# Kernel optimization log

Hardware: AMD Instinct MI355X
Metric: run time of the kernel (lower is better)

Reference implementation:

```python
import jax, jax.numpy as jnp
import numpy as np

N = 100000
E = 1600000
F = 64
THETA = (0.6, -0.4, 0.3, -0.2, 0.1)  # k = 5 polynomial coefficients


def setup_inputs() -> dict:
    key = jax.random.key(0)
    kx, ke = jax.random.split(key)
    x = jax.random.normal(kx, (N, F), dtype=jnp.float32)
    edge_index = jax.random.randint(ke, (2, E), 0, N, dtype=jnp.int64)
    return {"x": x, "edge_index": edge_index}


def _l_sym_mul(feat, src, dst, deg_inv_sqrt, n):
    # L_sym * feat = feat - D^{-1/2} A D^{-1/2} feat
    src_norm = feat[src] * deg_inv_sqrt[src]            # [E, F] gather + scale
    agg = jax.ops.segment_sum(src_norm, dst, num_segments=n)  # scatter-add to dst
    return feat - deg_inv_sqrt * agg


def reference(x, edge_index):
    src, dst = edge_index[0], edge_index[1]
    n = x.shape[0]
    # in-degree from dst, clamp to >= 1, D^{-1/2} as [N, 1]
    deg = jax.ops.segment_sum(jnp.ones((src.shape[0],), dtype=x.dtype), dst,
                              num_segments=n)
    deg = jnp.maximum(deg, 1.0)[:, None]
    deg_inv_sqrt = deg ** -0.5

    h_acc = THETA[0] * x
    feat = x
    for k in range(1, len(THETA)):
        feat = _l_sym_mul(feat, src, dst, deg_inv_sqrt, n)
        h_acc = h_acc + THETA[k] * feat
    return h_acc
```

## Files before the change

### kernel.cpp

```cpp
#include <hip/hip_runtime.h>


constexpr int kF = 64;
constexpr int BSHIFT = 8;
constexpr int NB = 1 << BSHIFT;
constexpr int TILE = 4096;
constexpr int KMAX = 512;

static __device__ __forceinline__ float bfl(unsigned u) {
    return __uint_as_float(u << 16);
}
static __device__ __forceinline__ float bfh(unsigned u) {
    return __uint_as_float(u & 0xffff0000u);
}
static __device__ __forceinline__ unsigned f2bf(float f) {
    unsigned u = __float_as_uint(f);
    return (u + 0x7fffu + ((u >> 16) & 1u)) >> 16;
}
static __device__ __forceinline__ unsigned pack2(float a, float b) {
    return f2bf(a) | (f2bf(b) << 16);
}

__global__ void k_binA(const int* __restrict__ src, const int* __restrict__ dst,
                       unsigned* __restrict__ pairs, int* __restrict__ gcursor,
                       const float4* __restrict__ x4, uint4* __restrict__ xb4,
                       int n8, int E, int K, int cap) {
    __shared__ int hist[KMAX];
    __shared__ int gb[KMAX];
    const int tid = threadIdx.x;
    const long long tb = (long long)blockIdx.x * TILE;
    const int tcount = (int)min((long long)TILE, (long long)E - tb);

    {
        int per = (n8 + gridDim.x - 1) / (int)gridDim.x;
        int b0 = blockIdx.x * per;
        int b1 = min(b0 + per, n8);
        for (int i = b0 + tid; i < b1; i += 512) {
            float4 a = x4[2 * i];
            float4 b = x4[2 * i + 1];
            uint4 o;
            o.x = pack2(a.x, a.y);
            o.y = pack2(a.z, a.w);
            o.z = pack2(b.x, b.y);
            o.w = pack2(b.z, b.w);
            xb4[i] = o;
        }
    }

    hist[tid] = 0;
    __syncthreads();
    for (int i = tid; i < tcount; i += 512)
        atomicAdd(&hist[dst[tb + i] >> BSHIFT], 1);
    __syncthreads();
    int hv = hist[tid];
    gb[tid] = (tid < K && hv > 0) ? atomicAdd(&gcursor[tid], hv) : 0;
    hist[tid] = 0;
    __syncthreads();
    for (int i = tid; i < tcount; i += 512) {
        int d = dst[tb + i];
        int s = src[tb + i];
        int b = d >> BSHIFT;
        int pos = atomicAdd(&hist[b], 1);
        pairs[(size_t)b * cap + gb[b] + pos] =
            ((unsigned)(d & (NB - 1)) << 23) | (unsigned)s;
    }
}

__global__ void k_binB1(const unsigned* __restrict__ pairs, const int* __restrict__ gcursor,
                        int* __restrict__ rp, float* __restrict__ dinv,
                        int N, int E, int K, int cap) {
    __shared__ int gsc[KMAX];
    __shared__ int cnt[NB];
    __shared__ int stmp[NB];
    const int b = blockIdx.x;
    const int tid = threadIdx.x;

    int gv = (tid < K) ? gcursor[tid] : 0;
    gsc[tid] = gv;
    __syncthreads();
    for (int o = 1; o < KMAX; o <<= 1) {
        int t = (tid >= o) ? gsc[tid - o] : 0;
        __syncthreads();
        gsc[tid] += t;
        __syncthreads();
    }
    const int ecnt = gcursor[b];
    const int base = gsc[b] - ecnt;
    const unsigned* bp = pairs + (size_t)b * cap;

    if (tid < NB) cnt[tid] = 0;
    __syncthreads();
    for (int i = tid; i < ecnt; i += 512)
        atomicAdd(&cnt[bp[i] >> 23], 1);
    __syncthreads();
    int v = (tid < NB) ? cnt[tid] : 0;
    if (tid < NB) stmp[tid] = v;
    __syncthreads();
    for (int o = 1; o < NB; o <<= 1) {
        int t = (tid >= o && tid < NB) ? stmp[tid - o] : 0;
        __syncthreads();
        if (tid < NB) stmp[tid] += t;
        __syncthreads();
    }
    int node = (b << BSHIFT) + tid;
    if (tid < NB && node < N) {
        rp[node] = base + stmp[tid] - v;
        dinv[node] = rsqrtf(fmaxf((float)v, 1.0f));
    }
    if (b == K - 1 && tid == 0) rp[N] = E;
}

__global__ void k_binB2(const unsigned* __restrict__ pairs, const int* __restrict__ gcursor,
                        const int* __restrict__ rp, const float* __restrict__ dinv,
                        int2* __restrict__ ecsr, int N, int K, int cap) {
    __shared__ int cur[NB];
    const int b = blockIdx.x;
    const int tid = threadIdx.x;
    const int ecnt = gcursor[b];
    const unsigned* bp = pairs + (size_t)b * cap;

    int node = (b << BSHIFT) + tid;
    if (tid < NB) cur[tid] = (node < N) ? rp[node] : 0;
    __syncthreads();
    for (int i = tid; i < ecnt; i += 512) {
        unsigned p = bp[i];
        int s = (int)(p & 0x7FFFFFu);
        int pos = atomicAdd(&cur[p >> 23], 1);
        ecsr[pos] = make_int2(s, __float_as_int(dinv[s]));
    }
}

__global__ void k_gather(const int* __restrict__ rp, const int2* __restrict__ ecsr,
                         const unsigned short* __restrict__ featin,
                         const float* __restrict__ dinv,
                         unsigned short* __restrict__ featout, int n) {
    int wid = (blockIdx.x * blockDim.x + threadIdx.x) >> 6;
    int lane = threadIdx.x & 63;
    int half = lane >> 5;
    int r = (lane >> 3) & 3;
    int c = lane & 7;
    int node = wid * 2 + half;
    if (wid * 2 >= n) return;
    bool valid = node < n;
    int beg = valid ? rp[node] : 0;
    int end = valid ? rp[node + 1] : 0;
    int len = end - beg;
    int olen = __shfl_xor(len, 32, 64);
    int mlen = (len > olen) ? len : olen;

    float acc[8] = {0.f, 0.f, 0.f, 0.f, 0.f, 0.f, 0.f, 0.f};
    for (int i = 0; i < mlen; i += 8) {
        int j1 = beg + i + r;
        int j2 = j1 + 4;
        bool ok1 = j1 < end;
        bool ok2 = j2 < end;
        int2 e1 = ecsr[ok1 ? j1 : 0];
        int2 e2 = ecsr[ok2 ? j2 : 0];
        int s1 = e1.x;
        int s2 = e2.x;
        float w1 = ok1 ? __int_as_float(e1.y) : 0.0f;
        float w2 = ok2 ? __int_as_float(e2.y) : 0.0f;
        uint4 ra = *(const uint4*)(featin + ((size_t)s1 << 6) + (c << 3));
        uint4 rb = *(const uint4*)(featin + ((size_t)s2 << 6) + (c << 3));
        acc[0] += w1 * bfl(ra.x);
        acc[1] += w1 * bfh(ra.x);
        acc[2] += w1 * bfl(ra.y);
        acc[3] += w1 * bfh(ra.y);
        acc[4] += w1 * bfl(ra.z);
        acc[5] += w1 * bfh(ra.z);
        acc[6] += w1 * bfl(ra.w);
        acc[7] += w1 * bfh(ra.w);
        acc[0] += w2 * bfl(rb.x);
        acc[1] += w2 * bfh(rb.x);
        acc[2] += w2 * bfl(rb.y);
        acc[3] += w2 * bfh(rb.y);
        acc[4] += w2 * bfl(rb.z);
        acc[5] += w2 * bfh(rb.z);
        acc[6] += w2 * bfl(rb.w);
        acc[7] += w2 * bfh(rb.w);
    }
    #pragma unroll
    for (int m = 8; m <= 16; m <<= 1) {
        #pragma unroll
        for (int i = 0; i < 8; ++i)
            acc[i] += __shfl_xor(acc[i], m, 64);
    }

    if (r == 0 && valid) {
        size_t off = ((size_t)node << 6) + (c << 3);
        uint4 rr = *(const uint4*)(featin + off);
        float di = dinv[node];
        uint4 o;
        o.x = pack2(bfl(rr.x) - di * acc[0], bfh(rr.x) - di * acc[1]);
        o.y = pack2(bfl(rr.y) - di * acc[2], bfh(rr.y) - di * acc[3]);
        o.z = pack2(bfl(rr.z) - di * acc[4], bfh(rr.z) - di * acc[5]);
        o.w = pack2(bfl(rr.w) - di * acc[6], bfh(rr.w) - di * acc[7]);
        *(uint4*)(featout + off) = o;
    }
}

__global__ void k_final(const float4* __restrict__ x4,
                        const uint4* __restrict__ f1, const uint4* __restrict__ f2,
                        const uint4* __restrict__ f3, const uint4* __restrict__ f4,
                        float4* __restrict__ h4, int n8,
                        float t0, float t1, float t2, float t3, float t4) {
    int i = blockIdx.x * blockDim.x + threadIdx.x;
    if (i >= n8) return;
    uint4 a = f1[i], b = f2[i], cc = f3[i], d = f4[i];
    float4 xa = x4[2 * i], xb = x4[2 * i + 1];
    float4 h0, h1;
    h0.x = t0 * xa.x + t1 * bfl(a.x) + t2 * bfl(b.x) + t3 * bfl(cc.x) + t4 * bfl(d.x);
    h0.y = t0 * xa.y + t1 * bfh(a.x) + t2 * bfh(b.x) + t3 * bfh(cc.x) + t4 * bfh(d.x);
    h0.z = t0 * xa.z + t1 * bfl(a.y) + t2 * bfl(b.y) + t3 * bfl(cc.y) + t4 * bfl(d.y);
    h0.w = t0 * xa.w + t1 * bfh(a.y) + t2 * bfh(b.y) + t3 * bfh(cc.y) + t4 * bfh(d.y);
    h1.x = t0 * xb.x + t1 * bfl(a.z) + t2 * bfl(b.z) + t3 * bfl(cc.z) + t4 * bfl(d.z);
    h1.y = t0 * xb.y + t1 * bfh(a.z) + t2 * bfh(b.z) + t3 * bfh(cc.z) + t4 * bfh(d.z);
    h1.z = t0 * xb.z + t1 * bfl(a.w) + t2 * bfl(b.w) + t3 * bfl(cc.w) + t4 * bfl(d.w);
    h1.w = t0 * xb.w + t1 * bfh(a.w) + t2 * bfh(b.w) + t3 * bfh(cc.w) + t4 * bfh(d.w);
    h4[2 * i] = h0;
    h4[2 * i + 1] = h1;
}

extern "C" void kernel_launch(void* const* d_in, const int* in_sizes, int n_in,
                              void* d_out, int out_size, void* d_ws, size_t ws_size,
                              hipStream_t stream) {
    const float* x  = (const float*)d_in[0];
    const int*   ei = (const int*)d_in[1];
    const int N = in_sizes[0] / kF;
    const int E = in_sizes[1] / 2;
    const int* src = ei;
    const int* dst = ei + E;
    float* h = (float*)d_out;

    const int K = (N + NB - 1) >> BSHIFT;
    const int cap = 2 * ((E + K - 1) / K);

    char* ws = (char*)d_ws;
    size_t off = 0;
    auto carve = [&](size_t bytes) {
        void* p = ws + off;
        off = (off + bytes + 511) & ~(size_t)511;
        return p;
    };
    int*            gcursor = (int*)carve((size_t)K * 4);
    int*            rp      = (int*)carve((size_t)(N + 1) * 4);
    float*          dinv    = (float*)carve((size_t)N * 4);
    int2*           ecsr    = (int2*)carve((size_t)E * 8);
    unsigned short* xb      = (unsigned short*)carve((size_t)N * kF * 2);
    unsigned short* f1      = (unsigned short*)carve((size_t)N * kF * 2);
    unsigned short* f2      = (unsigned short*)carve((size_t)N * kF * 2);
    unsigned short* f3      = (unsigned short*)carve((size_t)N * kF * 2);
    unsigned short* f4      = (unsigned short*)carve((size_t)N * kF * 2);
    unsigned*       pairs   = (unsigned*)carve((size_t)K * cap * 4);

    const float theta[5] = {0.6f, -0.4f, 0.3f, -0.2f, 0.1f};
    const int n8 = N * kF / 8;

    hipMemsetAsync(gcursor, 0, (size_t)K * 4, stream);
    k_binA<<<(E + TILE - 1) / TILE, 512, 0, stream>>>(src, dst, pairs, gcursor,
                                                      (const float4*)x, (uint4*)xb,
                                                      n8, E, K, cap);
    k_binB1<<<K, 512, 0, stream>>>(pairs, gcursor, rp, dinv, N, E, K, cap);
    k_binB2<<<K, 512, 0, stream>>>(pairs, gcursor, rp, dinv, ecsr, N, K, cap);

    const int nwaves = (N + 1) / 2;
    const int gblocks = (nwaves + 3) / 4;
    k_gather<<<gblocks, 256, 0, stream>>>(rp, ecsr, xb, dinv, f1, N);
    k_gather<<<gblocks, 256, 0, stream>>>(rp, ecsr, f1, dinv, f2, N);
    k_gather<<<gblocks, 256, 0, stream>>>(rp, ecsr, f2, dinv, f3, N);
    k_gather<<<gblocks, 256, 0, stream>>>(rp, ecsr, f3, dinv, f4, N);

    k_final<<<(n8 + 255) / 256, 256, 0, stream>>>((const float4*)x,
                                                  (const uint4*)f1, (const uint4*)f2,
                                                  (const uint4*)f3, (const uint4*)f4,
                                                  (float4*)h, n8,
                                                  theta[0], theta[1], theta[2],
                                                  theta[3], theta[4]);
}
```

Before: 274.6 us.

## Cache edge tiles in registers, unroll gather by four, read bf16 x in final

The binning kernel now uses a smaller tile (2048 edges) and holds each thread's four src/dst values in registers, so the second pass no longer re-reads them from global memory. The gather loop processes four edges per lane per iteration instead of two, putting more independent loads in flight. The final combine reads the bf16 copy of x instead of the fp32 input, which halves that read traffic but adds bf16 rounding error to the theta0*x term.

```diff
diff --git a/kernel.cpp b/kernel.cpp
--- a/kernel.cpp
+++ b/kernel.cpp
@@ -4,7 +4,7 @@
 constexpr int kF = 64;
 constexpr int BSHIFT = 8;
 constexpr int NB = 1 << BSHIFT;
-constexpr int TILE = 4096;
+constexpr int TILE = 2048;
 constexpr int KMAX = 512;
 
 static __device__ __forceinline__ float bfl(unsigned u) {
@@ -49,20 +49,32 @@
 
     hist[tid] = 0;
     __syncthreads();
-    for (int i = tid; i < tcount; i += 512)
-        atomicAdd(&hist[dst[tb + i] >> BSHIFT], 1);
+    int dc[4], sc[4];
+    #pragma unroll
+    for (int k = 0; k < 4; ++k) {
+        int i = tid + k * 512;
+        if (i < tcount) {
+            dc[k] = dst[tb + i];
+            sc[k] = src[tb + i];
+            atomicAdd(&hist[dc[k] >> BSHIFT], 1);
+        } else {
+            dc[k] = -1;
+        }
+    }
     __syncthreads();
     int hv = hist[tid];
     gb[tid] = (tid < K && hv > 0) ? atomicAdd(&gcursor[tid], hv) : 0;
     hist[tid] = 0;
     __syncthreads();
-    for (int i = tid; i < tcount; i += 512) {
-        int d = dst[tb + i];
-        int s = src[tb + i];
-        int b = d >> BSHIFT;
-        int pos = atomicAdd(&hist[b], 1);
-        pairs[(size_t)b * cap + gb[b] + pos] =
-            ((unsigned)(d & (NB - 1)) << 23) | (unsigned)s;
+    #pragma unroll
+    for (int k = 0; k < 4; ++k) {
+        if (dc[k] >= 0) {
+            int d = dc[k];
+            int b = d >> BSHIFT;
+            int pos = atomicAdd(&hist[b], 1);
+            pairs[(size_t)b * cap + gb[b] + pos] =
+                ((unsigned)(d & (NB - 1)) << 23) | (unsigned)sc[k];
+        }
     }
 }
 
@@ -149,35 +161,40 @@
     int mlen = (len > olen) ? len : olen;
 
     float acc[8] = {0.f, 0.f, 0.f, 0.f, 0.f, 0.f, 0.f, 0.f};
-    for (int i = 0; i < mlen; i += 8) {
+    for (int i = 0; i < mlen; i += 16) {
         int j1 = beg + i + r;
         int j2 = j1 + 4;
-        bool ok1 = j1 < end;
-        bool ok2 = j2 < end;
+        int j3 = j1 + 8;
+        int j4 = j1 + 12;
+        bool ok1 = j1 < end, ok2 = j2 < end, ok3 = j3 < end, ok4 = j4 < end;
         int2 e1 = ecsr[ok1 ? j1 : 0];
         int2 e2 = ecsr[ok2 ? j2 : 0];
-        int s1 = e1.x;
-        int s2 = e2.x;
+        int2 e3 = ecsr[ok3 ? j3 : 0];
+        int2 e4 = ecsr[ok4 ? j4 : 0];
         float w1 = ok1 ? __int_as_float(e1.y) : 0.0f;
         float w2 = ok2 ? __int_as_float(e2.y) : 0.0f;
-        uint4 ra = *(const uint4*)(featin + ((size_t)s1 << 6) + (c << 3));
-        uint4 rb = *(const uint4*)(featin + ((size_t)s2 << 6) + (c << 3));
-        acc[0] += w1 * bfl(ra.x);
-        acc[1] += w1 * bfh(ra.x);
-        acc[2] += w1 * bfl(ra.y);
-        acc[3] += w1 * bfh(ra.y);
-        acc[4] += w1 * bfl(ra.z);
-        acc[5] += w1 * bfh(ra.z);
-        acc[6] += w1 * bfl(ra.w);
-        acc[7] += w1 * bfh(ra.w);
-        acc[0] += w2 * bfl(rb.x);
-        acc[1] += w2 * bfh(rb.x);
-        acc[2] += w2 * bfl(rb.y);
-        acc[3] += w2 * bfh(rb.y);
-        acc[4] += w2 * bfl(rb.z);
-        acc[5] += w2 * bfh(rb.z);
-        acc[6] += w2 * bfl(rb.w);
-        acc[7] += w2 * bfh(rb.w);
+        float w3 = ok3 ? __int_as_float(e3.y) : 0.0f;
+        float w4 = ok4 ? __int_as_float(e4.y) : 0.0f;
+        uint4 ra = *(const uint4*)(featin + ((size_t)e1.x << 6) + (c << 3));
+        uint4 rb = *(const uint4*)(featin + ((size_t)e2.x << 6) + (c << 3));
+        uint4 rc = *(const uint4*)(featin + ((size_t)e3.x << 6) + (c << 3));
+        uint4 rd = *(const uint4*)(featin + ((size_t)e4.x << 6) + (c << 3));
+        acc[0] += w1 * bfl(ra.x); acc[1] += w1 * bfh(ra.x);
+        acc[2] += w1 * bfl(ra.y); acc[3] += w1 * bfh(ra.y);
+        acc[4] += w1 * bfl(ra.z); acc[5] += w1 * bfh(ra.z);
+        acc[6] += w1 * bfl(ra.w); acc[7] += w1 * bfh(ra.w);
+        acc[0] += w2 * bfl(rb.x); acc[1] += w2 * bfh(rb.x);
+        acc[2] += w2 * bfl(rb.y); acc[3] += w2 * bfh(rb.y);
+        acc[4] += w2 * bfl(rb.z); acc[5] += w2 * bfh(rb.z);
+        acc[6] += w2 * bfl(rb.w); acc[7] += w2 * bfh(rb.w);
+        acc[0] += w3 * bfl(rc.x); acc[1] += w3 * bfh(rc.x);
+        acc[2] += w3 * bfl(rc.y); acc[3] += w3 * bfh(rc.y);
+        acc[4] += w3 * bfl(rc.z); acc[5] += w3 * bfh(rc.z);
+        acc[6] += w3 * bfl(rc.w); acc[7] += w3 * bfh(rc.w);
+        acc[0] += w4 * bfl(rd.x); acc[1] += w4 * bfh(rd.x);
+        acc[2] += w4 * bfl(rd.y); acc[3] += w4 * bfh(rd.y);
+        acc[4] += w4 * bfl(rd.z); acc[5] += w4 * bfh(rd.z);
+        acc[6] += w4 * bfl(rd.w); acc[7] += w4 * bfh(rd.w);
     }
     #pragma unroll
     for (int m = 8; m <= 16; m <<= 1) {
@@ -199,24 +216,24 @@
     }
 }
 
-__global__ void k_final(const float4* __restrict__ x4,
+__global__ void k_final(const uint4* __restrict__ xb,
                         const uint4* __restrict__ f1, const uint4* __restrict__ f2,
                         const uint4* __restrict__ f3, const uint4* __restrict__ f4,
                         float4* __restrict__ h4, int n8,
                         float t0, float t1, float t2, float t3, float t4) {
     int i = blockIdx.x * blockDim.x + threadIdx.x;
     if (i >= n8) return;
+    uint4 xv = xb[i];
     uint4 a = f1[i], b = f2[i], cc = f3[i], d = f4[i];
-    float4 xa = x4[2 * i], xb = x4[2 * i + 1];
     float4 h0, h1;
-    h0.x = t0 * xa.x + t1 * bfl(a.x) + t2 * bfl(b.x) + t3 * bfl(cc.x) + t4 * bfl(d.x);
-    h0.y = t0 * xa.y + t1 * bfh(a.x) + t2 * bfh(b.x) + t3 * bfh(cc.x) + t4 * bfh(d.x);
-    h0.z = t0 * xa.z + t1 * bfl(a.y) + t2 * bfl(b.y) + t3 * bfl(cc.y) + t4 * bfl(d.y);
-    h0.w = t0 * xa.w + t1 * bfh(a.y) + t2 * bfh(b.y) + t3 * bfh(cc.y) + t4 * bfh(d.y);
-    h1.x = t0 * xb.x + t1 * bfl(a.z) + t2 * bfl(b.z) + t3 * bfl(cc.z) + t4 * bfl(d.z);
-    h1.y = t0 * xb.y + t1 * bfh(a.z) + t2 * bfh(b.z) + t3 * bfh(cc.z) + t4 * bfh(d.z);
-    h1.z = t0 * xb.z + t1 * bfl(a.w) + t2 * bfl(b.w) + t3 * bfl(cc.w) + t4 * bfl(d.w);
-    h1.w = t0 * xb.w + t1 * bfh(a.w) + t2 * bfh(b.w) + t3 * bfh(cc.w) + t4 * bfh(d.w);
+    h0.x = t0 * bfl(xv.x) + t1 * bfl(a.x) + t2 * bfl(b.x) + t3 * bfl(cc.x) + t4 * bfl(d.x);
+    h0.y = t0 * bfh(xv.x) + t1 * bfh(a.x) + t2 * bfh(b.x) + t3 * bfh(cc.x) + t4 * bfh(d.x);
+    h0.z = t0 * bfl(xv.y) + t1 * bfl(a.y) + t2 * bfl(b.y) + t3 * bfl(cc.y) + t4 * bfl(d.y);
+    h0.w = t0 * bfh(xv.y) + t1 * bfh(a.y) + t2 * bfh(b.y) + t3 * bfh(cc.y) + t4 * bfh(d.y);
+    h1.x = t0 * bfl(xv.z) + t1 * bfl(a.z) + t2 * bfl(b.z) + t3 * bfl(cc.z) + t4 * bfl(d.z);
+    h1.y = t0 * bfh(xv.z) + t1 * bfh(a.z) + t2 * bfh(b.z) + t3 * bfh(cc.z) + t4 * bfh(d.z);
+    h1.z = t0 * bfl(xv.w) + t1 * bfl(a.w) + t2 * bfl(b.w) + t3 * bfl(cc.w) + t4 * bfl(d.w);
+    h1.w = t0 * bfh(xv.w) + t1 * bfh(a.w) + t2 * bfh(b.w) + t3 * bfh(cc.w) + t4 * bfh(d.w);
     h4[2 * i] = h0;
     h4[2 * i + 1] = h1;
 }
@@ -270,7 +287,7 @@
     k_gather<<<gblocks, 256, 0, stream>>>(rp, ecsr, f2, dinv, f3, N);
     k_gather<<<gblocks, 256, 0, stream>>>(rp, ecsr, f3, dinv, f4, N);
 
-    k_final<<<(n8 + 255) / 256, 256, 0, stream>>>((const float4*)x,
+    k_final<<<(n8 + 255) / 256, 256, 0, stream>>>((const uint4*)xb,
                                                   (const uint4*)f1, (const uint4*)f2,
                                                   (const uint4*)f3, (const uint4*)f4,
                                                   (float4*)h, n8,
```

Measured after the change: 268.0 us. 2.4% less time.
